# Optimization experiments

Hardware: AMD Instinct MI355X
Metric: run time of the kernel (lower is better)

## Reference

```python
import jax, jax.numpy as jnp
import numpy as np

B, H, W, DIM, HEADS = 4, 32, 32, 768, 12
HD = DIM // HEADS


def setup_inputs() -> dict:
    key = jax.random.key(0)
    ks = jax.random.split(key, 5)
    return {
        "x": jax.random.normal(ks[0], (B, H, W, DIM), jnp.float32),
        "qkv_w": jax.random.normal(ks[1], (3 * DIM, DIM), jnp.float32) * 0.02,
        "qkv_b": jnp.zeros((3 * DIM,), jnp.float32),
        "proj_w": jax.random.normal(ks[2], (DIM, DIM), jnp.float32) * 0.02,
        "proj_b": jnp.zeros((DIM,), jnp.float32),
        "rel_pos_h": jax.random.normal(ks[3], (2 * H - 1, HD), jnp.float32) * 0.02,
        "rel_pos_w": jax.random.normal(ks[4], (2 * W - 1, HD), jnp.float32) * 0.02,
    }


def reference(x, qkv_w, qkv_b, proj_w, proj_b, rel_pos_h, rel_pos_w):
    b, h, w, dim = x.shape
    heads = HEADS
    hd = dim // heads
    n = h * w
    scale = hd ** -0.5

    xf = x.reshape(b, n, dim)
    qkv = xf @ qkv_w.T + qkv_b                          # [b, n, 3*dim]
    qkv = qkv.reshape(b, n, 3, heads, hd)
    qkv = jnp.transpose(qkv, (2, 0, 3, 1, 4)).reshape(3, b * heads, n, hd)
    q, k, v = qkv[0], qkv[1], qkv[2]                    # [b*heads, n, hd]

    # decomposed relative position bias (q_size == k_size, no interpolation)
    idx_h = jnp.arange(h)[:, None] - jnp.arange(h)[None, :] + (h - 1)
    idx_w = jnp.arange(w)[:, None] - jnp.arange(w)[None, :] + (w - 1)
    Rh = rel_pos_h[idx_h]                               # [h, h, hd]
    Rw = rel_pos_w[idx_w]                               # [w, w, hd]
    r_q = q.reshape(b * heads, h, w, hd)
    rel_h = jnp.einsum('bhwc,hkc->bhwk', r_q, Rh)       # [bH, h, w, h]
    rel_w = jnp.einsum('bhwc,wkc->bhwk', r_q, Rw)       # [bH, h, w, w]
    bias = (rel_h[:, :, :, :, None] + rel_w[:, :, :, None, :]).reshape(b * heads, n, n)

    attn = jax.nn.softmax(jnp.einsum('bnd,bmd->bnm', q * scale, k) + bias, axis=-1)
    out = jnp.einsum('bnm,bmd->bnd', attn, v)           # [b*heads, n, hd]
    out = out.reshape(b, heads, n, hd).transpose(0, 2, 1, 3).reshape(b, n, dim)
    out = out @ proj_w.T + proj_b
    return out.reshape(b, h, w, dim)
```

## Files before the change

kernel.cpp:

```cpp
#include <hip/hip_runtime.h>

#define DEV_INLINE static __device__ __forceinline__

typedef __attribute__((ext_vector_type(8))) short bf16x8;
typedef __attribute__((ext_vector_type(4))) float f32x4;
typedef __attribute__((ext_vector_type(16))) float f32x16;

DEV_INLINE unsigned short f2bf(float f) {
  union { float f; unsigned int u; } v; v.f = f;
  unsigned int u = v.u;
  u += 0x7FFFu + ((u >> 16) & 1u);
  return (unsigned short)(u >> 16);
}
DEV_INLINE float bf2f(unsigned short h) {
  union { unsigned int u; float f; } v; v.u = ((unsigned int)h) << 16; return v.f;
}

__global__ __launch_bounds__(256) void cvt_all(const float* __restrict__ x,
                                               const float* __restrict__ qw,
                                               const float* __restrict__ pw,
                                               unsigned short* __restrict__ xb,
                                               unsigned short* __restrict__ wqkv,
                                               unsigned short* __restrict__ wproj) {
  const int bid = blockIdx.x;
  const float* in;
  unsigned short* out;
  int i;
  if (bid < 3072)      { in = x;  out = xb;    i = bid * 256 + threadIdx.x; }
  else if (bid < 4800) { in = qw; out = wqkv;  i = (bid - 3072) * 256 + threadIdx.x; }
  else                 { in = pw; out = wproj; i = (bid - 4800) * 256 + threadIdx.x; }
  float4 v = reinterpret_cast<const float4*>(in)[i];
  ushort4 o;
  o.x = f2bf(v.x); o.y = f2bf(v.y); o.z = f2bf(v.z); o.w = f2bf(v.w);
  reinterpret_cast<ushort4*>(out)[i] = o;
}

template <int MODE>
__global__ __launch_bounds__(256) void gemm_bf16(const unsigned short* __restrict__ A,
                                                 const unsigned short* __restrict__ Bw,
                                                 const float* __restrict__ bias,
                                                 float* __restrict__ outF,
                                                 unsigned short* __restrict__ qo,
                                                 unsigned short* __restrict__ ko,
                                                 unsigned short* __restrict__ vo) {
  __shared__ unsigned short As[3][128 * 32];
  __shared__ unsigned short Bs[3][128 * 32];

  const int tid = threadIdx.x;
  const int lane = tid & 63;
  const int wv = tid >> 6;
  const int wrow = (wv >> 1) * 64;
  const int wcol = (wv & 1) * 64;
  const int m0 = blockIdx.y * 128;
  const int n0 = blockIdx.x * 128;
  const int l15 = lane & 15;
  const int lg = lane >> 4;

  const int srow = lane >> 2;
  const int seg  = (lane & 3) ^ (srow & 3);

  f32x4 acc[4][4];
#pragma unroll
  for (int i = 0; i < 4; ++i)
#pragma unroll
    for (int j = 0; j < 4; ++j) acc[i][j] = (f32x4){0.f, 0.f, 0.f, 0.f};

#define GSTAGE(KT, B)                                                                        \
  do {                                                                                       \
    _Pragma("unroll") for (int pp = 0; pp < 2; ++pp) {                                       \
      int p = wv * 2 + pp;                                   \
      int row = p * 16 + srow;                                                               \
      const unsigned short* ga = &A[(m0 + row) * 768 + (KT) * 32 + seg * 8];                 \
      __builtin_amdgcn_global_load_lds(                                                      \
          (const __attribute__((address_space(1))) unsigned int*)ga,                         \
          (__attribute__((address_space(3))) unsigned int*)&As[B][p * 512], 16, 0, 0);       \
      const unsigned short* gb = &Bw[(n0 + row) * 768 + (KT) * 32 + seg * 8];                \
      __builtin_amdgcn_global_load_lds(                                                      \
          (const __attribute__((address_space(1))) unsigned int*)gb,                         \
          (__attribute__((address_space(3))) unsigned int*)&Bs[B][p * 512], 16, 0, 0);       \
    }                                                                                        \
  } while (0)

  GSTAGE(0, 0);
  GSTAGE(1, 1);

  const int soff = (lg ^ (l15 & 3)) * 8;

#pragma unroll
  for (int kt = 0; kt < 24; ++kt) {
    const int b = kt % 3;
    if (kt < 23) asm volatile("s_waitcnt vmcnt(4)" ::: "memory");
    else         asm volatile("s_waitcnt vmcnt(0)" ::: "memory");
    __builtin_amdgcn_s_barrier();
    asm volatile("" ::: "memory");
    if (kt < 22) GSTAGE(kt + 2, (kt + 2) % 3);

    bf16x8 aF[4], bF[4];
#pragma unroll
    for (int i = 0; i < 4; ++i)
      aF[i] = *reinterpret_cast<const bf16x8*>(&As[b][(wrow + i * 16 + l15) * 32 + soff]);
#pragma unroll
    for (int j = 0; j < 4; ++j)
      bF[j] = *reinterpret_cast<const bf16x8*>(&Bs[b][(wcol + j * 16 + l15) * 32 + soff]);
#pragma unroll
    for (int i = 0; i < 4; ++i)
#pragma unroll
      for (int j = 0; j < 4; ++j)
        acc[i][j] = __builtin_amdgcn_mfma_f32_16x16x32_bf16(aF[i], bF[j], acc[i][j], 0, 0, 0);
  }
#undef GSTAGE

#pragma unroll
  for (int i = 0; i < 4; ++i) {
#pragma unroll
    for (int j = 0; j < 4; ++j) {
#pragma unroll
      for (int r = 0; r < 4; ++r) {
        int row = m0 + wrow + i * 16 + (lane >> 4) * 4 + r;
        int col = n0 + wcol + j * 16 + l15;
        float val = acc[i][j][r] + bias[col];
        if (MODE == 0) {
          int t = col / 768;
          int rem = col - t * 768;
          int head = rem >> 6;
          int c = rem & 63;
          int bb = row >> 10;
          int n = row & 1023;
          if (t == 0) val *= 1.44269504f;
          if (t == 1) val *= 0.125f;
          unsigned short* dst = (t == 0) ? qo : (t == 1) ? ko : vo;
          dst[((bb * 12 + head) * 1024 + n) * 64 + c] = f2bf(val);
        } else {
          outF[row * 768 + col] = val;
        }
      }
    }
  }
}

__global__ __launch_bounds__(256) void vtrans(const unsigned short* __restrict__ vb,
                                              unsigned short* __restrict__ vt) {
  __shared__ unsigned short t[64][72];
  const int n0 = blockIdx.x * 64;
  const int bh = blockIdx.y;
  const int tid = threadIdx.x;
#pragma unroll
  for (int i = 0; i < 4; ++i) {
    int s = tid + i * 256;
    int row = s >> 4, c4 = (s & 15) * 4;
    *reinterpret_cast<ushort4*>(&t[row][c4]) =
        *reinterpret_cast<const ushort4*>(&vb[(bh * 1024 + n0 + row) * 64 + c4]);
  }
  __syncthreads();
#pragma unroll
  for (int i = 0; i < 4; ++i) {
    int s = tid + i * 256;
    int d = s >> 4, n4 = (s & 15) * 4;
    ushort4 o;
    o.x = t[n4 + 0][d]; o.y = t[n4 + 1][d]; o.z = t[n4 + 2][d]; o.w = t[n4 + 3][d];
    *reinterpret_cast<ushort4*>(&vt[(bh * 64 + d) * 1024 + n0 + n4]) = o;
  }
}

DEV_INLINE f32x4 mfma16(bf16x8 a, bf16x8 b, f32x4 c) {
  return __builtin_amdgcn_mfma_f32_16x16x32_bf16(a, b, c, 0, 0, 0);
}

__global__ __launch_bounds__(64) void rel_mfma16(const unsigned short* __restrict__ q,
                                                 const float* __restrict__ rph,
                                                 const float* __restrict__ rpw,
                                                 unsigned short* __restrict__ relwb,
                                                 float* __restrict__ relh) {
  __shared__ unsigned short qs[32 * 72];
  __shared__ unsigned short rhh[32 * 72], rhl[32 * 72];
  __shared__ unsigned short rwh[64 * 72], rwl[64 * 72];
  __shared__ float relh_s[32 * 36];
  __shared__ unsigned short relw_s[32 * 40];

  const int lane = threadIdx.x;
  const int l15 = lane & 15;
  const int lg = lane >> 4;
  const int qh = blockIdx.x;
  const int bh = blockIdx.y;

#pragma unroll
  for (int it = 0; it < 4; ++it) {
    int s = lane + it * 64;
    int row = s >> 3, ch = s & 7;
    *reinterpret_cast<int4*>(&qs[row * 72 + ch * 8]) =
        *reinterpret_cast<const int4*>(&q[(bh * 1024 + qh * 32 + row) * 64 + ch * 8]);
  }
#pragma unroll
  for (int it = 0; it < 8; ++it) {
    int s = lane + it * 64;
    int row = s >> 4, c4 = (s & 15) * 4;
    float4 v = *reinterpret_cast<const float4*>(&rph[(qh + row) * 64 + c4]);
    ushort4 h, l;
    h.x = f2bf(v.x); l.x = f2bf(v.x - bf2f(h.x));
    h.y = f2bf(v.y); l.y = f2bf(v.y - bf2f(h.y));
    h.z = f2bf(v.z); l.z = f2bf(v.z - bf2f(h.z));
    h.w = f2bf(v.w); l.w = f2bf(v.w - bf2f(h.w));
    *reinterpret_cast<ushort4*>(&rhh[row * 72 + c4]) = h;
    *reinterpret_cast<ushort4*>(&rhl[row * 72 + c4]) = l;
  }
#pragma unroll
  for (int it = 0; it < 16; ++it) {
    int s = lane + it * 64;
    int row = s >> 4, c4 = (s & 15) * 4;
    float4 v = (float4){0.f, 0.f, 0.f, 0.f};
    if (row < 63) v = *reinterpret_cast<const float4*>(&rpw[row * 64 + c4]);
    ushort4 h, l;
    h.x = f2bf(v.x); l.x = f2bf(v.x - bf2f(h.x));
    h.y = f2bf(v.y); l.y = f2bf(v.y - bf2f(h.y));
    h.z = f2bf(v.z); l.z = f2bf(v.z - bf2f(h.z));
    h.w = f2bf(v.w); l.w = f2bf(v.w - bf2f(h.w));
    *reinterpret_cast<ushort4*>(&rwh[row * 72 + c4]) = h;
    *reinterpret_cast<ushort4*>(&rwl[row * 72 + c4]) = l;
  }
  __syncthreads();

  const int k0 = lg * 8, k1 = 32 + lg * 8;
  bf16x8 fq[2][2], fhh[2][2], fhl[2][2], fwh[4][2], fwl[4][2];
#pragma unroll
  for (int t = 0; t < 2; ++t) {
    fq[t][0]  = *reinterpret_cast<const bf16x8*>(&qs[(t * 16 + l15) * 72 + k0]);
    fq[t][1]  = *reinterpret_cast<const bf16x8*>(&qs[(t * 16 + l15) * 72 + k1]);
    fhh[t][0] = *reinterpret_cast<const bf16x8*>(&rhh[(t * 16 + l15) * 72 + k0]);
    fhh[t][1] = *reinterpret_cast<const bf16x8*>(&rhh[(t * 16 + l15) * 72 + k1]);
    fhl[t][0] = *reinterpret_cast<const bf16x8*>(&rhl[(t * 16 + l15) * 72 + k0]);
    fhl[t][1] = *reinterpret_cast<const bf16x8*>(&rhl[(t * 16 + l15) * 72 + k1]);
  }
#pragma unroll
  for (int t = 0; t < 4; ++t) {
    fwh[t][0] = *reinterpret_cast<const bf16x8*>(&rwh[(t * 16 + l15) * 72 + k0]);
    fwh[t][1] = *reinterpret_cast<const bf16x8*>(&rwh[(t * 16 + l15) * 72 + k1]);
    fwl[t][0] = *reinterpret_cast<const bf16x8*>(&rwl[(t * 16 + l15) * 72 + k0]);
    fwl[t][1] = *reinterpret_cast<const bf16x8*>(&rwl[(t * 16 + l15) * 72 + k1]);
  }

  f32x4 ah[2][2];
#pragma unroll
  for (int i = 0; i < 2; ++i)
#pragma unroll
    for (int jj = 0; jj < 2; ++jj) {
      f32x4 a = (f32x4){0.f, 0.f, 0.f, 0.f};
      a = mfma16(fhh[i][0], fq[jj][0], a);
      a = mfma16(fhh[i][1], fq[jj][1], a);
      a = mfma16(fhl[i][0], fq[jj][0], a);
      a = mfma16(fhl[i][1], fq[jj][1], a);
      ah[i][jj] = a;
    }
  f32x4 aw[2][4];
#pragma unroll
  for (int i = 0; i < 2; ++i)
#pragma unroll
    for (int jj = 0; jj < 4; ++jj) {
      f32x4 a = (f32x4){0.f, 0.f, 0.f, 0.f};
      a = mfma16(fq[i][0], fwh[jj][0], a);
      a = mfma16(fq[i][1], fwh[jj][1], a);
      a = mfma16(fq[i][0], fwl[jj][0], a);
      a = mfma16(fq[i][1], fwl[jj][1], a);
      aw[i][jj] = a;
    }

#pragma unroll
  for (int i = 0; i < 2; ++i)
#pragma unroll
    for (int jj = 0; jj < 2; ++jj)
#pragma unroll
      for (int r = 0; r < 4; ++r) {
        int t = i * 16 + lg * 4 + r;
        int qw = jj * 16 + l15;
        relh_s[qw * 36 + 31 - t] = ah[i][jj][r];
      }
#pragma unroll
  for (int i = 0; i < 2; ++i)
#pragma unroll
    for (int jj = 0; jj < 4; ++jj)
#pragma unroll
      for (int r = 0; r < 4; ++r) {
        int qw = i * 16 + lg * 4 + r;
        int d = jj * 16 + l15;
        int kw = qw + 31 - d;
        if (kw >= 0 && kw < 32) relw_s[qw * 40 + kw] = f2bf(aw[i][jj][r]);
      }
  __syncthreads();

#pragma unroll
  for (int it = 0; it < 4; ++it) {
    int s = lane + it * 64;
    int row = s >> 3, c4 = (s & 7) * 4;
    *reinterpret_cast<float4*>(&relh[(bh * 1024 + qh * 32 + row) * 32 + c4]) =
        *reinterpret_cast<const float4*>(&relh_s[row * 36 + c4]);
  }
#pragma unroll
  for (int it = 0; it < 2; ++it) {
    int s = lane + it * 64;
    int row = s >> 2, ch = s & 3;
    *reinterpret_cast<int4*>(&relwb[(bh * 1024 + qh * 32 + row) * 32 + ch * 8]) =
        *reinterpret_cast<const int4*>(&relw_s[row * 40 + ch * 8]);
  }
}

DEV_INLINE f32x16 mfma32(bf16x8 a, bf16x8 b, f32x16 c) {
  return __builtin_amdgcn_mfma_f32_32x32x16_bf16(a, b, c, 0, 0, 0);
}

DEV_INLINE bf16x8 make_pa(const float* p) {
  unsigned int W0, W1, W2, W3;
  asm("v_cvt_pk_bf16_f32 %0, %1, %2" : "=v"(W0) : "v"(p[0]), "v"(p[1]));
  asm("v_cvt_pk_bf16_f32 %0, %1, %2" : "=v"(W1) : "v"(p[2]), "v"(p[3]));
  asm("v_cvt_pk_bf16_f32 %0, %1, %2" : "=v"(W2) : "v"(p[4]), "v"(p[5]));
  asm("v_cvt_pk_bf16_f32 %0, %1, %2" : "=v"(W3) : "v"(p[6]), "v"(p[7]));
  asm("v_permlane32_swap_b32 %0, %1" : "+v"(W0), "+v"(W2));
  asm("v_permlane32_swap_b32 %0, %1" : "+v"(W1), "+v"(W3));
  union { unsigned int w[4]; bf16x8 v; } u;
  u.w[0] = W0; u.w[1] = W1; u.w[2] = W2; u.w[3] = W3;
  return u.v;
}

__global__ __launch_bounds__(128) void attn2(const unsigned short* __restrict__ kg,
                                             const unsigned short* __restrict__ vtg,
                                             const unsigned short* __restrict__ qg,
                                             const unsigned short* __restrict__ relwb,
                                             const float* __restrict__ relh,
                                             unsigned short* __restrict__ ao) {
  __shared__ unsigned short k_lin[3][64 * 64];
  __shared__ unsigned short v_lin[3][64 * 64];

  const int tid = threadIdx.x;
  const int lane = tid & 63;
  const int wv = tid >> 6;
  const int l31 = lane & 31;
  const int hi = lane >> 5;

  const int bid = blockIdx.x;
  const int swz = (bid & 7) * 96 + (bid >> 3);
  const int bh = swz >> 4;
  const int qt = swz & 15;
  const int q0 = qt * 64 + wv * 32;

  bf16x8 qf[6];
  {
    const unsigned short* qrow = &qg[(bh * 1024 + q0 + l31) * 64 + hi * 8];
#pragma unroll
    for (int c = 0; c < 4; ++c)
      qf[c] = *reinterpret_cast<const bf16x8*>(&qrow[c * 16]);
    const unsigned short* wrow = &relwb[(bh * 1024 + q0 + l31) * 32 + hi * 8];
    qf[4] = *reinterpret_cast<const bf16x8*>(&wrow[0]);
    qf[5] = *reinterpret_cast<const bf16x8*>(&wrow[16]);
  }

  bf16x8 ohf0, ohf1;
  {
    int t0 = l31 - 8 * hi;
    int t1 = l31 - 16 - 8 * hi;
    union { unsigned int w[4]; bf16x8 v; } u0, u1;
#pragma unroll
    for (int w = 0; w < 4; ++w) {
      u0.w[w] = (t0 >= 0 && (t0 >> 1) == w) ? ((t0 & 1) ? 0x3F800000u : 0x3F80u) : 0u;
      u1.w[w] = (t1 >= 0 && (t1 >> 1) == w) ? ((t1 & 1) ? 0x3F800000u : 0x3F80u) : 0u;
    }
    ohf0 = u0.v; ohf1 = u1.v;
  }

  f32x16 O0, O1;
#pragma unroll
  for (int r = 0; r < 16; ++r) { O0[r] = 0.f; O1[r] = 0.f; }
  float m_r = -3.0e38f, l_r = 0.f;

  const int srow = lane >> 3;
  const int scb = (lane & 7) ^ srow;
  const int rsw = l31 & 7;

#define STAGE(KT, B)                                                                       \
  do {                                                                                     \
    _Pragma("unroll") for (int pp = 0; pp < 4; ++pp) {                                     \
      int p = wv * 4 + pp;                                                                 \
      int row = p * 8 + srow;                                                              \
      const unsigned short* gk = &kg[(bh * 1024 + (KT) * 64 + row) * 64 + scb * 8];        \
      __builtin_amdgcn_global_load_lds(                                                    \
          (const __attribute__((address_space(1))) unsigned int*)gk,                       \
          (__attribute__((address_space(3))) unsigned int*)&k_lin[B][p * 512], 16, 0, 0);  \
      const unsigned short* gv = &vtg[(bh * 64 + row) * 1024 + (KT) * 64 + scb * 8];       \
      __builtin_amdgcn_global_load_lds(                                                    \
          (const __attribute__((address_space(1))) unsigned int*)gv,                       \
          (__attribute__((address_space(3))) unsigned int*)&v_lin[B][p * 512], 16, 0, 0);  \
    }                                                                                      \
  } while (0)

  STAGE(0, 0);
  STAGE(1, 1);

  const float* rhrow = &relh[(bh * 1024 + q0 + l31) * 32];
  float2 bhv = *reinterpret_cast<const float2*>(&rhrow[0]);

  for (int kt = 0; kt < 16; ++kt) {
    const int b = kt % 3;
    if (kt < 15) asm volatile("s_waitcnt vmcnt(8)" ::: "memory");
    else         asm volatile("s_waitcnt vmcnt(0)" ::: "memory");
    __builtin_amdgcn_s_barrier();
    asm volatile("" ::: "memory");
    if (kt < 14) STAGE(kt + 2, (kt + 2) % 3);

    float2 bhv_next = bhv;
    if (kt < 15) bhv_next = *reinterpret_cast<const float2*>(&rhrow[2 * (kt + 1)]);
    float bh0 = bhv.x, bh1 = bhv.y;

    f32x16 s0, s1;
#pragma unroll
    for (int r = 0; r < 16; ++r) { s0[r] = 0.f; s1[r] = 0.f; }
    {
      const unsigned short* kb0 = &k_lin[b][l31 * 64];
      const unsigned short* kb1 = &k_lin[b][(32 + l31) * 64];
      __builtin_amdgcn_s_setprio(1);
#pragma unroll
      for (int c = 0; c < 4; ++c) {
        int cb = ((2 * c + hi) ^ rsw) * 8;
        s0 = mfma32(*reinterpret_cast<const bf16x8*>(&kb0[cb]), qf[c], s0);
        s1 = mfma32(*reinterpret_cast<const bf16x8*>(&kb1[cb]), qf[c], s1);
      }
      s0 = mfma32(ohf0, qf[4], s0);
      s0 = mfma32(ohf1, qf[5], s0);
      s1 = mfma32(ohf0, qf[4], s1);
      s1 = mfma32(ohf1, qf[5], s1);
      __builtin_amdgcn_s_setprio(0);
    }

    float pm0 = s0[0], pm1 = s1[0];
#pragma unroll
    for (int r = 1; r < 16; ++r) { pm0 = fmaxf(pm0, s0[r]); pm1 = fmaxf(pm1, s1[r]); }
    float pmax = fmaxf(pm0 + bh0, pm1 + bh1);
    pmax = fmaxf(pmax, __shfl_xor(pmax, 32));

    if (!__all(pmax <= m_r + 11.5f)) {
      float mnew = fmaxf(m_r, pmax);
      float corr = __builtin_amdgcn_exp2f(m_r - mnew);
      m_r = mnew;
      l_r *= corr;
#pragma unroll
      for (int r = 0; r < 16; ++r) {
        int cr = ((r & 3) + 8 * (r >> 2) + 4 * hi) << 2;
        float c2 = __int_as_float(__builtin_amdgcn_ds_bpermute(cr, __float_as_int(corr)));
        O0[r] *= c2;
        O1[r] *= c2;
      }
    }

    float mb0 = m_r - bh0, mb1 = m_r - bh1;
    float p0[16], p1[16];
    float ps = 0.f;
#pragma unroll
    for (int r = 0; r < 16; ++r) { p0[r] = __builtin_amdgcn_exp2f(s0[r] - mb0); ps += p0[r]; }
#pragma unroll
    for (int r = 0; r < 16; ++r) { p1[r] = __builtin_amdgcn_exp2f(s1[r] - mb1); ps += p1[r]; }
    ps += __shfl_xor(ps, 32);
    l_r += ps;

    bf16x8 pa0 = make_pa(p0 + 0);
    bf16x8 pa1 = make_pa(p0 + 8);
    bf16x8 pa2 = make_pa(p1 + 0);
    bf16x8 pa3 = make_pa(p1 + 8);

    const unsigned short* vb0 = &v_lin[b][l31 * 64];
    const unsigned short* vb1 = &v_lin[b][(32 + l31) * 64];
    __builtin_amdgcn_s_setprio(1);
#pragma unroll
    for (int c = 0; c < 4; ++c) {
      bf16x8 pac = (c == 0) ? pa0 : (c == 1) ? pa1 : (c == 2) ? pa2 : pa3;
      int cb = ((2 * c + hi) ^ rsw) * 8;
      O0 = mfma32(pac, *reinterpret_cast<const bf16x8*>(&vb0[cb]), O0);
      O1 = mfma32(pac, *reinterpret_cast<const bf16x8*>(&vb1[cb]), O1);
    }
    __builtin_amdgcn_s_setprio(0);

    bhv = bhv_next;
  }
#undef STAGE

  float invl = 1.f / l_r;
  const int bb = bh / 12, head = bh % 12;
#pragma unroll
  for (int r = 0; r < 16; ++r) {
    int crow = (r & 3) + 8 * (r >> 2) + 4 * hi;
    float il = __int_as_float(__builtin_amdgcn_ds_bpermute(crow << 2, __float_as_int(invl)));
    int n = q0 + crow;
    unsigned short* dst = &ao[(bb * 1024 + n) * 768 + head * 64];
    dst[l31] = f2bf(O0[r] * il);
    dst[32 + l31] = f2bf(O1[r] * il);
  }
}

extern "C" void kernel_launch(void* const* d_in, const int* in_sizes, int n_in,
                              void* d_out, int out_size, void* d_ws, size_t ws_size,
                              hipStream_t stream) {
  const float* x      = (const float*)d_in[0];
  const float* qkv_w  = (const float*)d_in[1];
  const float* qkv_b  = (const float*)d_in[2];
  const float* proj_w = (const float*)d_in[3];
  const float* proj_b = (const float*)d_in[4];
  const float* rph    = (const float*)d_in[5];
  const float* rpw    = (const float*)d_in[6];
  float* out = (float*)d_out;

  char* ws = (char*)d_ws;
  unsigned short* xb    = (unsigned short*)(ws);
  float*          relh  = (float*)(ws);
  unsigned short* wqkv  = (unsigned short*)(ws + 6291456);
  unsigned short* wproj = (unsigned short*)(ws + 9830400);
  unsigned short* qb    = (unsigned short*)(ws + 11010048);
  unsigned short* kb    = (unsigned short*)(ws + 17301504);
  unsigned short* vb    = (unsigned short*)(ws + 23592960);
  unsigned short* ao    = (unsigned short*)(ws + 23592960);
  unsigned short* vt    = (unsigned short*)(ws + 29884416);
  unsigned short* relwb = (unsigned short*)(ws + 36175872);

  cvt_all<<<5376, 256, 0, stream>>>(x, qkv_w, proj_w, xb, wqkv, wproj);

  gemm_bf16<0><<<dim3(18, 32), 256, 0, stream>>>(xb, wqkv, qkv_b, nullptr, qb, kb, vb);
  vtrans<<<dim3(16, 48), 256, 0, stream>>>(vb, vt);
  rel_mfma16<<<dim3(32, 48), 64, 0, stream>>>(qb, rph, rpw, relwb, relh);
  attn2<<<768, 128, 0, stream>>>(kb, vt, qb, relwb, relh, ao);
  gemm_bf16<1><<<dim3(6, 32), 256, 0, stream>>>(ao, wproj, proj_b, out, nullptr, nullptr, nullptr);
}
```

Before: 110.1 us.

## Software-pipeline QK^T of next tile ahead of softmax in attention loop

Restructures the attention loop so the QK^T MFMAs for tile kt+1 are issued before the softmax and PV work of tile kt. The aim is to overlap matrix-core work with the exp and reduction VALU work. Max and sum reductions become balanced trees to shorten dependency chains. The fine-grained vmcnt(8) waits are replaced by full __syncthreads. This may shrink the effective prefetch depth, and the last iteration does one redundant QK^T.

```diff
diff --git a/kernel.cpp b/kernel.cpp
--- a/kernel.cpp
+++ b/kernel.cpp
@@ -319,6 +319,23 @@
   return u.v;
 }
 
+DEV_INLINE float tree_max16(const float* s) {
+  float a0 = fmaxf(s[0], s[1]),  a1 = fmaxf(s[2], s[3]);
+  float a2 = fmaxf(s[4], s[5]),  a3 = fmaxf(s[6], s[7]);
+  float a4 = fmaxf(s[8], s[9]),  a5 = fmaxf(s[10], s[11]);
+  float a6 = fmaxf(s[12], s[13]), a7 = fmaxf(s[14], s[15]);
+  float b0 = fmaxf(a0, a1), b1 = fmaxf(a2, a3), b2 = fmaxf(a4, a5), b3 = fmaxf(a6, a7);
+  return fmaxf(fmaxf(b0, b1), fmaxf(b2, b3));
+}
+DEV_INLINE float tree_sum16(const float* s) {
+  float a0 = s[0] + s[1],  a1 = s[2] + s[3];
+  float a2 = s[4] + s[5],  a3 = s[6] + s[7];
+  float a4 = s[8] + s[9],  a5 = s[10] + s[11];
+  float a6 = s[12] + s[13], a7 = s[14] + s[15];
+  float b0 = a0 + a1, b1 = a2 + a3, b2 = a4 + a5, b3 = a6 + a7;
+  return (b0 + b1) + (b2 + b3);
+}
+
 __global__ __launch_bounds__(128) void attn2(const unsigned short* __restrict__ kg,
                                              const unsigned short* __restrict__ vtg,
                                              const unsigned short* __restrict__ qg,
@@ -389,47 +406,48 @@
     }                                                                                      \
   } while (0)
 
+#define QKT(BUF, S0, S1)                                                                   \
+  do {                                                                                     \
+    const unsigned short* kb0 = &k_lin[BUF][l31 * 64];                                     \
+    const unsigned short* kb1 = &k_lin[BUF][(32 + l31) * 64];                              \
+    _Pragma("unroll") for (int r = 0; r < 16; ++r) { S0[r] = 0.f; S1[r] = 0.f; }           \
+    __builtin_amdgcn_s_setprio(1);                                                         \
+    _Pragma("unroll") for (int c = 0; c < 4; ++c) {                                        \
+      int cb = ((2 * c + hi) ^ rsw) * 8;                                                   \
+      S0 = mfma32(*reinterpret_cast<const bf16x8*>(&kb0[cb]), qf[c], S0);                  \
+      S1 = mfma32(*reinterpret_cast<const bf16x8*>(&kb1[cb]), qf[c], S1);                  \
+    }                                                                                      \
+    S0 = mfma32(ohf0, qf[4], S0);                                                          \
+    S0 = mfma32(ohf1, qf[5], S0);                                                          \
+    S1 = mfma32(ohf0, qf[4], S1);                                                          \
+    S1 = mfma32(ohf1, qf[5], S1);                                                          \
+    __builtin_amdgcn_s_setprio(0);                                                         \
+  } while (0)
+
   STAGE(0, 0);
   STAGE(1, 1);
+  __syncthreads();
 
   const float* rhrow = &relh[(bh * 1024 + q0 + l31) * 32];
   float2 bhv = *reinterpret_cast<const float2*>(&rhrow[0]);
 
+  f32x16 sc0, sc1;
+  QKT(0, sc0, sc1);
+
   for (int kt = 0; kt < 16; ++kt) {
-    const int b = kt % 3;
-    if (kt < 15) asm volatile("s_waitcnt vmcnt(8)" ::: "memory");
-    else         asm volatile("s_waitcnt vmcnt(0)" ::: "memory");
-    __builtin_amdgcn_s_barrier();
-    asm volatile("" ::: "memory");
+    __syncthreads();
     if (kt < 14) STAGE(kt + 2, (kt + 2) % 3);
 
     float2 bhv_next = bhv;
     if (kt < 15) bhv_next = *reinterpret_cast<const float2*>(&rhrow[2 * (kt + 1)]);
     float bh0 = bhv.x, bh1 = bhv.y;
 
-    f32x16 s0, s1;
-#pragma unroll
-    for (int r = 0; r < 16; ++r) { s0[r] = 0.f; s1[r] = 0.f; }
-    {
-      const unsigned short* kb0 = &k_lin[b][l31 * 64];
-      const unsigned short* kb1 = &k_lin[b][(32 + l31) * 64];
-      __builtin_amdgcn_s_setprio(1);
-#pragma unroll
-      for (int c = 0; c < 4; ++c) {
-        int cb = ((2 * c + hi) ^ rsw) * 8;
-        s0 = mfma32(*reinterpret_cast<const bf16x8*>(&kb0[cb]), qf[c], s0);
-        s1 = mfma32(*reinterpret_cast<const bf16x8*>(&kb1[cb]), qf[c], s1);
-      }
-      s0 = mfma32(ohf0, qf[4], s0);
-      s0 = mfma32(ohf1, qf[5], s0);
-      s1 = mfma32(ohf0, qf[4], s1);
-      s1 = mfma32(ohf1, qf[5], s1);
-      __builtin_amdgcn_s_setprio(0);
-    }
-
-    float pm0 = s0[0], pm1 = s1[0];
-#pragma unroll
-    for (int r = 1; r < 16; ++r) { pm0 = fmaxf(pm0, s0[r]); pm1 = fmaxf(pm1, s1[r]); }
+    const int nb = (kt < 15 ? kt + 1 : 15) % 3;
+    f32x16 sn0, sn1;
+    QKT(nb, sn0, sn1);
+
+    float pm0 = tree_max16((const float*)&sc0);
+    float pm1 = tree_max16((const float*)&sc1);
     float pmax = fmaxf(pm0 + bh0, pm1 + bh1);
     pmax = fmaxf(pmax, __shfl_xor(pmax, 32));
 
@@ -449,11 +467,11 @@
 
     float mb0 = m_r - bh0, mb1 = m_r - bh1;
     float p0[16], p1[16];
-    float ps = 0.f;
-#pragma unroll
-    for (int r = 0; r < 16; ++r) { p0[r] = __builtin_amdgcn_exp2f(s0[r] - mb0); ps += p0[r]; }
-#pragma unroll
-    for (int r = 0; r < 16; ++r) { p1[r] = __builtin_amdgcn_exp2f(s1[r] - mb1); ps += p1[r]; }
+#pragma unroll
+    for (int r = 0; r < 16; ++r) p0[r] = __builtin_amdgcn_exp2f(sc0[r] - mb0);
+#pragma unroll
+    for (int r = 0; r < 16; ++r) p1[r] = __builtin_amdgcn_exp2f(sc1[r] - mb1);
+    float ps = tree_sum16(p0) + tree_sum16(p1);
     ps += __shfl_xor(ps, 32);
     l_r += ps;
 
@@ -462,8 +480,9 @@
     bf16x8 pa2 = make_pa(p1 + 0);
     bf16x8 pa3 = make_pa(p1 + 8);
 
-    const unsigned short* vb0 = &v_lin[b][l31 * 64];
-    const unsigned short* vb1 = &v_lin[b][(32 + l31) * 64];
+    const int vbuf = kt % 3;
+    const unsigned short* vb0 = &v_lin[vbuf][l31 * 64];
+    const unsigned short* vb1 = &v_lin[vbuf][(32 + l31) * 64];
     __builtin_amdgcn_s_setprio(1);
 #pragma unroll
     for (int c = 0; c < 4; ++c) {
@@ -474,8 +493,11 @@
     }
     __builtin_amdgcn_s_setprio(0);
 
+    sc0 = sn0;
+    sc1 = sn1;
     bhv = bhv_next;
   }
+#undef QKT
 #undef STAGE
 
   float invl = 1.f / l_r;
```

Result: no change. 110.8 us (+0.6%).

## Split attention KV range across two wave pairs and merge partial softmax in LDS

Applied to the files above, without the earlier changes.

Each attention block now runs four waves instead of two. Two waves cover the first half of the key tiles and two cover the second half, each with its own double-buffered LDS staging. The partial max, sum and output from the second half are written to shared memory and merged in a flash-decoding style combine. This halves the serial key loop per wave to raise latency hiding and occupancy, at the cost of a reduction epilogue, extra barriers, and replacing the 3-stage vmcnt pipeline with a simpler __syncthreads double buffer. Max and sum reductions are also rewritten as balanced trees to shorten dependency chains.

```diff
diff --git a/kernel.cpp b/kernel.cpp
--- a/kernel.cpp
+++ b/kernel.cpp
@@ -319,18 +319,37 @@
   return u.v;
 }
 
-__global__ __launch_bounds__(128) void attn2(const unsigned short* __restrict__ kg,
+DEV_INLINE float tree_max16(const float* s) {
+  float a0 = fmaxf(s[0], s[1]),  a1 = fmaxf(s[2], s[3]);
+  float a2 = fmaxf(s[4], s[5]),  a3 = fmaxf(s[6], s[7]);
+  float a4 = fmaxf(s[8], s[9]),  a5 = fmaxf(s[10], s[11]);
+  float a6 = fmaxf(s[12], s[13]), a7 = fmaxf(s[14], s[15]);
+  float b0 = fmaxf(a0, a1), b1 = fmaxf(a2, a3), b2 = fmaxf(a4, a5), b3 = fmaxf(a6, a7);
+  return fmaxf(fmaxf(b0, b1), fmaxf(b2, b3));
+}
+DEV_INLINE float tree_sum16(const float* s) {
+  float a0 = s[0] + s[1],  a1 = s[2] + s[3];
+  float a2 = s[4] + s[5],  a3 = s[6] + s[7];
+  float a4 = s[8] + s[9],  a5 = s[10] + s[11];
+  float a6 = s[12] + s[13], a7 = s[14] + s[15];
+  float b0 = a0 + a1, b1 = a2 + a3, b2 = a4 + a5, b3 = a6 + a7;
+  return (b0 + b1) + (b2 + b3);
+}
+
+__global__ __launch_bounds__(256) void attn2(const unsigned short* __restrict__ kg,
                                              const unsigned short* __restrict__ vtg,
                                              const unsigned short* __restrict__ qg,
                                              const unsigned short* __restrict__ relwb,
                                              const float* __restrict__ relh,
                                              unsigned short* __restrict__ ao) {
-  __shared__ unsigned short k_lin[3][64 * 64];
-  __shared__ unsigned short v_lin[3][64 * 64];
+  __shared__ unsigned short k_lin[2][2][64 * 64];
+  __shared__ unsigned short v_lin[2][2][64 * 64];
 
   const int tid = threadIdx.x;
   const int lane = tid & 63;
   const int wv = tid >> 6;
+  const int qh2 = wv & 1;
+  const int kvh = wv >> 1;
   const int l31 = lane & 31;
   const int hi = lane >> 5;
 
@@ -338,7 +357,7 @@
   const int swz = (bid & 7) * 96 + (bid >> 3);
   const int bh = swz >> 4;
   const int qt = swz & 15;
-  const int q0 = qt * 64 + wv * 32;
+  const int q0 = qt * 64 + qh2 * 32;
 
   bf16x8 qf[6];
   {
@@ -373,46 +392,43 @@
   const int scb = (lane & 7) ^ srow;
   const int rsw = l31 & 7;
 
-#define STAGE(KT, B)                                                                       \
-  do {                                                                                     \
-    _Pragma("unroll") for (int pp = 0; pp < 4; ++pp) {                                     \
-      int p = wv * 4 + pp;                                                                 \
-      int row = p * 8 + srow;                                                              \
-      const unsigned short* gk = &kg[(bh * 1024 + (KT) * 64 + row) * 64 + scb * 8];        \
-      __builtin_amdgcn_global_load_lds(                                                    \
-          (const __attribute__((address_space(1))) unsigned int*)gk,                       \
-          (__attribute__((address_space(3))) unsigned int*)&k_lin[B][p * 512], 16, 0, 0);  \
-      const unsigned short* gv = &vtg[(bh * 64 + row) * 1024 + (KT) * 64 + scb * 8];       \
-      __builtin_amdgcn_global_load_lds(                                                    \
-          (const __attribute__((address_space(1))) unsigned int*)gv,                       \
-          (__attribute__((address_space(3))) unsigned int*)&v_lin[B][p * 512], 16, 0, 0);  \
-    }                                                                                      \
+#define STAGE(KT, B)                                                                            \
+  do {                                                                                          \
+    _Pragma("unroll") for (int pp = 0; pp < 4; ++pp) {                                          \
+      int p = qh2 * 4 + pp;                                                                     \
+      int row = p * 8 + srow;                                                                   \
+      const unsigned short* gk = &kg[(bh * 1024 + (KT) * 64 + row) * 64 + scb * 8];             \
+      __builtin_amdgcn_global_load_lds(                                                         \
+          (const __attribute__((address_space(1))) unsigned int*)gk,                            \
+          (__attribute__((address_space(3))) unsigned int*)&k_lin[kvh][B][p * 512], 16, 0, 0);  \
+      const unsigned short* gv = &vtg[(bh * 64 + row) * 1024 + (KT) * 64 + scb * 8];            \
+      __builtin_amdgcn_global_load_lds(                                                         \
+          (const __attribute__((address_space(1))) unsigned int*)gv,                            \
+          (__attribute__((address_space(3))) unsigned int*)&v_lin[kvh][B][p * 512], 16, 0, 0);  \
+    }                                                                                           \
   } while (0)
 
-  STAGE(0, 0);
-  STAGE(1, 1);
+  const int kt0 = kvh * 8;
+  STAGE(kt0, 0);
 
   const float* rhrow = &relh[(bh * 1024 + q0 + l31) * 32];
-  float2 bhv = *reinterpret_cast<const float2*>(&rhrow[0]);
-
-  for (int kt = 0; kt < 16; ++kt) {
-    const int b = kt % 3;
-    if (kt < 15) asm volatile("s_waitcnt vmcnt(8)" ::: "memory");
-    else         asm volatile("s_waitcnt vmcnt(0)" ::: "memory");
-    __builtin_amdgcn_s_barrier();
-    asm volatile("" ::: "memory");
-    if (kt < 14) STAGE(kt + 2, (kt + 2) % 3);
+  float2 bhv = *reinterpret_cast<const float2*>(&rhrow[2 * kt0]);
+
+  for (int lt = 0; lt < 8; ++lt) {
+    const int b = lt & 1;
+    __syncthreads();
+    if (lt < 7) STAGE(kt0 + lt + 1, b ^ 1);
 
     float2 bhv_next = bhv;
-    if (kt < 15) bhv_next = *reinterpret_cast<const float2*>(&rhrow[2 * (kt + 1)]);
+    if (lt < 7) bhv_next = *reinterpret_cast<const float2*>(&rhrow[2 * (kt0 + lt + 1)]);
     float bh0 = bhv.x, bh1 = bhv.y;
 
     f32x16 s0, s1;
 #pragma unroll
     for (int r = 0; r < 16; ++r) { s0[r] = 0.f; s1[r] = 0.f; }
     {
-      const unsigned short* kb0 = &k_lin[b][l31 * 64];
-      const unsigned short* kb1 = &k_lin[b][(32 + l31) * 64];
+      const unsigned short* kb0 = &k_lin[kvh][b][l31 * 64];
+      const unsigned short* kb1 = &k_lin[kvh][b][(32 + l31) * 64];
       __builtin_amdgcn_s_setprio(1);
 #pragma unroll
       for (int c = 0; c < 4; ++c) {
@@ -427,9 +443,8 @@
       __builtin_amdgcn_s_setprio(0);
     }
 
-    float pm0 = s0[0], pm1 = s1[0];
-#pragma unroll
-    for (int r = 1; r < 16; ++r) { pm0 = fmaxf(pm0, s0[r]); pm1 = fmaxf(pm1, s1[r]); }
+    float pm0 = tree_max16((const float*)&s0);
+    float pm1 = tree_max16((const float*)&s1);
     float pmax = fmaxf(pm0 + bh0, pm1 + bh1);
     pmax = fmaxf(pmax, __shfl_xor(pmax, 32));
 
@@ -449,11 +464,11 @@
 
     float mb0 = m_r - bh0, mb1 = m_r - bh1;
     float p0[16], p1[16];
-    float ps = 0.f;
-#pragma unroll
-    for (int r = 0; r < 16; ++r) { p0[r] = __builtin_amdgcn_exp2f(s0[r] - mb0); ps += p0[r]; }
-#pragma unroll
-    for (int r = 0; r < 16; ++r) { p1[r] = __builtin_amdgcn_exp2f(s1[r] - mb1); ps += p1[r]; }
+#pragma unroll
+    for (int r = 0; r < 16; ++r) p0[r] = __builtin_amdgcn_exp2f(s0[r] - mb0);
+#pragma unroll
+    for (int r = 0; r < 16; ++r) p1[r] = __builtin_amdgcn_exp2f(s1[r] - mb1);
+    float ps = tree_sum16(p0) + tree_sum16(p1);
     ps += __shfl_xor(ps, 32);
     l_r += ps;
 
@@ -462,8 +477,8 @@
     bf16x8 pa2 = make_pa(p1 + 0);
     bf16x8 pa3 = make_pa(p1 + 8);
 
-    const unsigned short* vb0 = &v_lin[b][l31 * 64];
-    const unsigned short* vb1 = &v_lin[b][(32 + l31) * 64];
+    const unsigned short* vb0 = &v_lin[kvh][b][l31 * 64];
+    const unsigned short* vb1 = &v_lin[kvh][b][(32 + l31) * 64];
     __builtin_amdgcn_s_setprio(1);
 #pragma unroll
     for (int c = 0; c < 4; ++c) {
@@ -478,16 +493,39 @@
   }
 #undef STAGE
 
-  float invl = 1.f / l_r;
-  const int bb = bh / 12, head = bh % 12;
-#pragma unroll
-  for (int r = 0; r < 16; ++r) {
-    int crow = (r & 3) + 8 * (r >> 2) + 4 * hi;
-    float il = __int_as_float(__builtin_amdgcn_ds_bpermute(crow << 2, __float_as_int(invl)));
-    int n = q0 + crow;
-    unsigned short* dst = &ao[(bb * 1024 + n) * 768 + head * 64];
-    dst[l31] = f2bf(O0[r] * il);
-    dst[32 + l31] = f2bf(O1[r] * il);
+  __syncthreads();
+  float* mb = reinterpret_cast<float*>(&k_lin[0][0][0]);
+  const int base = (qh2 * 64 + lane) * 34;
+  if (kvh == 1) {
+    mb[base + 0] = m_r;
+    mb[base + 1] = l_r;
+#pragma unroll
+    for (int r = 0; r < 16; ++r) { mb[base + 2 + r] = O0[r]; mb[base + 18 + r] = O1[r]; }
+  }
+  __syncthreads();
+  if (kvh == 0) {
+    float m_o = mb[base + 0], l_o = mb[base + 1];
+    float mn = fmaxf(m_r, m_o);
+    float ca = __builtin_amdgcn_exp2f(m_r - mn);
+    float cb = __builtin_amdgcn_exp2f(m_o - mn);
+    l_r = l_r * ca + l_o * cb;
+    float invl = 1.f / l_r;
+
+    const int bb = bh / 12, head = bh % 12;
+#pragma unroll
+    for (int r = 0; r < 16; ++r) {
+      int crow = (r & 3) + 8 * (r >> 2) + 4 * hi;
+      int cri = crow << 2;
+      float car = __int_as_float(__builtin_amdgcn_ds_bpermute(cri, __float_as_int(ca)));
+      float cbr = __int_as_float(__builtin_amdgcn_ds_bpermute(cri, __float_as_int(cb)));
+      float il  = __int_as_float(__builtin_amdgcn_ds_bpermute(cri, __float_as_int(invl)));
+      float o0 = (O0[r] * car + mb[base + 2 + r] * cbr) * il;
+      float o1 = (O1[r] * car + mb[base + 18 + r] * cbr) * il;
+      int n = q0 + crow;
+      unsigned short* dst = &ao[(bb * 1024 + n) * 768 + head * 64];
+      dst[l31] = f2bf(o0);
+      dst[32 + l31] = f2bf(o1);
+    }
   }
 }
 
@@ -520,6 +558,6 @@
   gemm_bf16<0><<<dim3(18, 32), 256, 0, stream>>>(xb, wqkv, qkv_b, nullptr, qb, kb, vb);
   vtrans<<<dim3(16, 48), 256, 0, stream>>>(vb, vt);
   rel_mfma16<<<dim3(32, 48), 64, 0, stream>>>(qb, rph, rpw, relwb, relh);
-  attn2<<<768, 128, 0, stream>>>(kb, vt, qb, relwb, relh, ao);
+  attn2<<<768, 256, 0, stream>>>(kb, vt, qb, relwb, relh, ao);
   gemm_bf16<1><<<dim3(6, 32), 256, 0, stream>>>(ao, wproj, proj_b, out, nullptr, nullptr, nullptr);
 }
```

New measurement: 112.2 us. About the same (+1.9%).

## Run attention block as one wave handling two 32-row query tiles

Applied to the files above, without the earlier changes.

The attention kernel moves from two waves per 64-query block to a single wave that processes both 32-row query halves in turn, reusing each staged K/V tile from LDS. With one wave per block the workgroup barrier goes away, and that wave issues all the global-to-LDS staging loads itself. In exchange the kernel holds twice the accumulators and Q fragments in registers, which may lower occupancy. The grid also has half as many waves, so there is less parallelism to hide latency.

```diff
diff --git a/kernel.cpp b/kernel.cpp
--- a/kernel.cpp
+++ b/kernel.cpp
@@ -319,18 +319,83 @@
   return u.v;
 }
 
-__global__ __launch_bounds__(128) void attn2(const unsigned short* __restrict__ kg,
-                                             const unsigned short* __restrict__ vtg,
-                                             const unsigned short* __restrict__ qg,
-                                             const unsigned short* __restrict__ relwb,
-                                             const float* __restrict__ relh,
-                                             unsigned short* __restrict__ ao) {
+DEV_INLINE void attn_tile(const unsigned short* kb0, const unsigned short* kb1,
+                          const unsigned short* vb0, const unsigned short* vb1,
+                          const bf16x8* qf, bf16x8 ohf0, bf16x8 ohf1,
+                          int hi, int rsw, float bh0, float bh1,
+                          f32x16& O0, f32x16& O1, float& m_r, float& l_r) {
+  f32x16 s0, s1;
+#pragma unroll
+  for (int r = 0; r < 16; ++r) { s0[r] = 0.f; s1[r] = 0.f; }
+  __builtin_amdgcn_s_setprio(1);
+#pragma unroll
+  for (int c = 0; c < 4; ++c) {
+    int cb = ((2 * c + hi) ^ rsw) * 8;
+    s0 = mfma32(*reinterpret_cast<const bf16x8*>(&kb0[cb]), qf[c], s0);
+    s1 = mfma32(*reinterpret_cast<const bf16x8*>(&kb1[cb]), qf[c], s1);
+  }
+  s0 = mfma32(ohf0, qf[4], s0);
+  s0 = mfma32(ohf1, qf[5], s0);
+  s1 = mfma32(ohf0, qf[4], s1);
+  s1 = mfma32(ohf1, qf[5], s1);
+  __builtin_amdgcn_s_setprio(0);
+
+  float pm0 = s0[0], pm1 = s1[0];
+#pragma unroll
+  for (int r = 1; r < 16; ++r) { pm0 = fmaxf(pm0, s0[r]); pm1 = fmaxf(pm1, s1[r]); }
+  float pmax = fmaxf(pm0 + bh0, pm1 + bh1);
+  pmax = fmaxf(pmax, __shfl_xor(pmax, 32));
+
+  if (!__all(pmax <= m_r + 11.5f)) {
+    float mnew = fmaxf(m_r, pmax);
+    float corr = __builtin_amdgcn_exp2f(m_r - mnew);
+    m_r = mnew;
+    l_r *= corr;
+#pragma unroll
+    for (int r = 0; r < 16; ++r) {
+      int cr = ((r & 3) + 8 * (r >> 2) + 4 * hi) << 2;
+      float c2 = __int_as_float(__builtin_amdgcn_ds_bpermute(cr, __float_as_int(corr)));
+      O0[r] *= c2;
+      O1[r] *= c2;
+    }
+  }
+
+  float mb0 = m_r - bh0, mb1 = m_r - bh1;
+  float p0[16], p1[16];
+  float ps = 0.f;
+#pragma unroll
+  for (int r = 0; r < 16; ++r) { p0[r] = __builtin_amdgcn_exp2f(s0[r] - mb0); ps += p0[r]; }
+#pragma unroll
+  for (int r = 0; r < 16; ++r) { p1[r] = __builtin_amdgcn_exp2f(s1[r] - mb1); ps += p1[r]; }
+  ps += __shfl_xor(ps, 32);
+  l_r += ps;
+
+  bf16x8 pa0 = make_pa(p0 + 0);
+  bf16x8 pa1 = make_pa(p0 + 8);
+  bf16x8 pa2 = make_pa(p1 + 0);
+  bf16x8 pa3 = make_pa(p1 + 8);
+
+  __builtin_amdgcn_s_setprio(1);
+#pragma unroll
+  for (int c = 0; c < 4; ++c) {
+    bf16x8 pac = (c == 0) ? pa0 : (c == 1) ? pa1 : (c == 2) ? pa2 : pa3;
+    int cb = ((2 * c + hi) ^ rsw) * 8;
+    O0 = mfma32(pac, *reinterpret_cast<const bf16x8*>(&vb0[cb]), O0);
+    O1 = mfma32(pac, *reinterpret_cast<const bf16x8*>(&vb1[cb]), O1);
+  }
+  __builtin_amdgcn_s_setprio(0);
+}
+
+__global__ __launch_bounds__(64) void attn2(const unsigned short* __restrict__ kg,
+                                            const unsigned short* __restrict__ vtg,
+                                            const unsigned short* __restrict__ qg,
+                                            const unsigned short* __restrict__ relwb,
+                                            const float* __restrict__ relh,
+                                            unsigned short* __restrict__ ao) {
   __shared__ unsigned short k_lin[3][64 * 64];
   __shared__ unsigned short v_lin[3][64 * 64];
 
-  const int tid = threadIdx.x;
-  const int lane = tid & 63;
-  const int wv = tid >> 6;
+  const int lane = threadIdx.x;
   const int l31 = lane & 31;
   const int hi = lane >> 5;
 
@@ -338,17 +403,23 @@
   const int swz = (bid & 7) * 96 + (bid >> 3);
   const int bh = swz >> 4;
   const int qt = swz & 15;
-  const int q0 = qt * 64 + wv * 32;
-
-  bf16x8 qf[6];
+  const int q0 = qt * 64;
+
+  bf16x8 qfA[6], qfB[6];
   {
-    const unsigned short* qrow = &qg[(bh * 1024 + q0 + l31) * 64 + hi * 8];
-#pragma unroll
-    for (int c = 0; c < 4; ++c)
-      qf[c] = *reinterpret_cast<const bf16x8*>(&qrow[c * 16]);
-    const unsigned short* wrow = &relwb[(bh * 1024 + q0 + l31) * 32 + hi * 8];
-    qf[4] = *reinterpret_cast<const bf16x8*>(&wrow[0]);
-    qf[5] = *reinterpret_cast<const bf16x8*>(&wrow[16]);
+    const unsigned short* qrowA = &qg[(bh * 1024 + q0 + l31) * 64 + hi * 8];
+    const unsigned short* qrowB = &qg[(bh * 1024 + q0 + 32 + l31) * 64 + hi * 8];
+#pragma unroll
+    for (int c = 0; c < 4; ++c) {
+      qfA[c] = *reinterpret_cast<const bf16x8*>(&qrowA[c * 16]);
+      qfB[c] = *reinterpret_cast<const bf16x8*>(&qrowB[c * 16]);
+    }
+    const unsigned short* wrowA = &relwb[(bh * 1024 + q0 + l31) * 32 + hi * 8];
+    const unsigned short* wrowB = &relwb[(bh * 1024 + q0 + 32 + l31) * 32 + hi * 8];
+    qfA[4] = *reinterpret_cast<const bf16x8*>(&wrowA[0]);
+    qfA[5] = *reinterpret_cast<const bf16x8*>(&wrowA[16]);
+    qfB[4] = *reinterpret_cast<const bf16x8*>(&wrowB[0]);
+    qfB[5] = *reinterpret_cast<const bf16x8*>(&wrowB[16]);
   }
 
   bf16x8 ohf0, ohf1;
@@ -364,10 +435,10 @@
     ohf0 = u0.v; ohf1 = u1.v;
   }
 
-  f32x16 O0, O1;
-#pragma unroll
-  for (int r = 0; r < 16; ++r) { O0[r] = 0.f; O1[r] = 0.f; }
-  float m_r = -3.0e38f, l_r = 0.f;
+  f32x16 OA0, OA1, OB0, OB1;
+#pragma unroll
+  for (int r = 0; r < 16; ++r) { OA0[r] = 0.f; OA1[r] = 0.f; OB0[r] = 0.f; OB1[r] = 0.f; }
+  float mA = -3.0e38f, lA = 0.f, mB = -3.0e38f, lB = 0.f;
 
   const int srow = lane >> 3;
   const int scb = (lane & 7) ^ srow;
@@ -375,119 +446,76 @@
 
 #define STAGE(KT, B)                                                                       \
   do {                                                                                     \
-    _Pragma("unroll") for (int pp = 0; pp < 4; ++pp) {                                     \
-      int p = wv * 4 + pp;                                                                 \
-      int row = p * 8 + srow;                                                              \
+    _Pragma("unroll") for (int pp = 0; pp < 8; ++pp) {                                     \
+      int row = pp * 8 + srow;                                                             \
       const unsigned short* gk = &kg[(bh * 1024 + (KT) * 64 + row) * 64 + scb * 8];        \
       __builtin_amdgcn_global_load_lds(                                                    \
           (const __attribute__((address_space(1))) unsigned int*)gk,                       \
-          (__attribute__((address_space(3))) unsigned int*)&k_lin[B][p * 512], 16, 0, 0);  \
+          (__attribute__((address_space(3))) unsigned int*)&k_lin[B][pp * 512], 16, 0, 0); \
       const unsigned short* gv = &vtg[(bh * 64 + row) * 1024 + (KT) * 64 + scb * 8];       \
       __builtin_amdgcn_global_load_lds(                                                    \
           (const __attribute__((address_space(1))) unsigned int*)gv,                       \
-          (__attribute__((address_space(3))) unsigned int*)&v_lin[B][p * 512], 16, 0, 0);  \
+          (__attribute__((address_space(3))) unsigned int*)&v_lin[B][pp * 512], 16, 0, 0); \
     }                                                                                      \
   } while (0)
 
   STAGE(0, 0);
   STAGE(1, 1);
 
-  const float* rhrow = &relh[(bh * 1024 + q0 + l31) * 32];
-  float2 bhv = *reinterpret_cast<const float2*>(&rhrow[0]);
+  const float* rhrowA = &relh[(bh * 1024 + q0 + l31) * 32];
+  const float* rhrowB = &relh[(bh * 1024 + q0 + 32 + l31) * 32];
+  float2 bhvA = *reinterpret_cast<const float2*>(&rhrowA[0]);
+  float2 bhvB = *reinterpret_cast<const float2*>(&rhrowB[0]);
 
   for (int kt = 0; kt < 16; ++kt) {
     const int b = kt % 3;
-    if (kt < 15) asm volatile("s_waitcnt vmcnt(8)" ::: "memory");
+    if (kt < 15) asm volatile("s_waitcnt vmcnt(16)" ::: "memory");
     else         asm volatile("s_waitcnt vmcnt(0)" ::: "memory");
-    __builtin_amdgcn_s_barrier();
-    asm volatile("" ::: "memory");
     if (kt < 14) STAGE(kt + 2, (kt + 2) % 3);
 
-    float2 bhv_next = bhv;
-    if (kt < 15) bhv_next = *reinterpret_cast<const float2*>(&rhrow[2 * (kt + 1)]);
-    float bh0 = bhv.x, bh1 = bhv.y;
-
-    f32x16 s0, s1;
-#pragma unroll
-    for (int r = 0; r < 16; ++r) { s0[r] = 0.f; s1[r] = 0.f; }
-    {
-      const unsigned short* kb0 = &k_lin[b][l31 * 64];
-      const unsigned short* kb1 = &k_lin[b][(32 + l31) * 64];
-      __builtin_amdgcn_s_setprio(1);
-#pragma unroll
-      for (int c = 0; c < 4; ++c) {
-        int cb = ((2 * c + hi) ^ rsw) * 8;
-        s0 = mfma32(*reinterpret_cast<const bf16x8*>(&kb0[cb]), qf[c], s0);
-        s1 = mfma32(*reinterpret_cast<const bf16x8*>(&kb1[cb]), qf[c], s1);
-      }
-      s0 = mfma32(ohf0, qf[4], s0);
-      s0 = mfma32(ohf1, qf[5], s0);
-      s1 = mfma32(ohf0, qf[4], s1);
-      s1 = mfma32(ohf1, qf[5], s1);
-      __builtin_amdgcn_s_setprio(0);
-    }
-
-    float pm0 = s0[0], pm1 = s1[0];
-#pragma unroll
-    for (int r = 1; r < 16; ++r) { pm0 = fmaxf(pm0, s0[r]); pm1 = fmaxf(pm1, s1[r]); }
-    float pmax = fmaxf(pm0 + bh0, pm1 + bh1);
-    pmax = fmaxf(pmax, __shfl_xor(pmax, 32));
-
-    if (!__all(pmax <= m_r + 11.5f)) {
-      float mnew = fmaxf(m_r, pmax);
-      float corr = __builtin_amdgcn_exp2f(m_r - mnew);
-      m_r = mnew;
-      l_r *= corr;
-#pragma unroll
-      for (int r = 0; r < 16; ++r) {
-        int cr = ((r & 3) + 8 * (r >> 2) + 4 * hi) << 2;
-        float c2 = __int_as_float(__builtin_amdgcn_ds_bpermute(cr, __float_as_int(corr)));
-        O0[r] *= c2;
-        O1[r] *= c2;
-      }
-    }
-
-    float mb0 = m_r - bh0, mb1 = m_r - bh1;
-    float p0[16], p1[16];
-    float ps = 0.f;
-#pragma unroll
-    for (int r = 0; r < 16; ++r) { p0[r] = __builtin_amdgcn_exp2f(s0[r] - mb0); ps += p0[r]; }
-#pragma unroll
-    for (int r = 0; r < 16; ++r) { p1[r] = __builtin_amdgcn_exp2f(s1[r] - mb1); ps += p1[r]; }
-    ps += __shfl_xor(ps, 32);
-    l_r += ps;
-
-    bf16x8 pa0 = make_pa(p0 + 0);
-    bf16x8 pa1 = make_pa(p0 + 8);
-    bf16x8 pa2 = make_pa(p1 + 0);
-    bf16x8 pa3 = make_pa(p1 + 8);
-
+    float2 bhvA_next = bhvA, bhvB_next = bhvB;
+    if (kt < 15) {
+      bhvA_next = *reinterpret_cast<const float2*>(&rhrowA[2 * (kt + 1)]);
+      bhvB_next = *reinterpret_cast<const float2*>(&rhrowB[2 * (kt + 1)]);
+    }
+
+    const unsigned short* kb0 = &k_lin[b][l31 * 64];
+    const unsigned short* kb1 = &k_lin[b][(32 + l31) * 64];
     const unsigned short* vb0 = &v_lin[b][l31 * 64];
     const unsigned short* vb1 = &v_lin[b][(32 + l31) * 64];
-    __builtin_amdgcn_s_setprio(1);
-#pragma unroll
-    for (int c = 0; c < 4; ++c) {
-      bf16x8 pac = (c == 0) ? pa0 : (c == 1) ? pa1 : (c == 2) ? pa2 : pa3;
-      int cb = ((2 * c + hi) ^ rsw) * 8;
-      O0 = mfma32(pac, *reinterpret_cast<const bf16x8*>(&vb0[cb]), O0);
-      O1 = mfma32(pac, *reinterpret_cast<const bf16x8*>(&vb1[cb]), O1);
-    }
-    __builtin_amdgcn_s_setprio(0);
-
-    bhv = bhv_next;
+
+    attn_tile(kb0, kb1, vb0, vb1, qfA, ohf0, ohf1, hi, rsw, bhvA.x, bhvA.y, OA0, OA1, mA, lA);
+    attn_tile(kb0, kb1, vb0, vb1, qfB, ohf0, ohf1, hi, rsw, bhvB.x, bhvB.y, OB0, OB1, mB, lB);
+
+    bhvA = bhvA_next;
+    bhvB = bhvB_next;
   }
 #undef STAGE
 
-  float invl = 1.f / l_r;
   const int bb = bh / 12, head = bh % 12;
-#pragma unroll
-  for (int r = 0; r < 16; ++r) {
-    int crow = (r & 3) + 8 * (r >> 2) + 4 * hi;
-    float il = __int_as_float(__builtin_amdgcn_ds_bpermute(crow << 2, __float_as_int(invl)));
-    int n = q0 + crow;
-    unsigned short* dst = &ao[(bb * 1024 + n) * 768 + head * 64];
-    dst[l31] = f2bf(O0[r] * il);
-    dst[32 + l31] = f2bf(O1[r] * il);
+  {
+    float invl = 1.f / lA;
+#pragma unroll
+    for (int r = 0; r < 16; ++r) {
+      int crow = (r & 3) + 8 * (r >> 2) + 4 * hi;
+      float il = __int_as_float(__builtin_amdgcn_ds_bpermute(crow << 2, __float_as_int(invl)));
+      int n = q0 + crow;
+      unsigned short* dst = &ao[(bb * 1024 + n) * 768 + head * 64];
+      dst[l31] = f2bf(OA0[r] * il);
+      dst[32 + l31] = f2bf(OA1[r] * il);
+    }
+  }
+  {
+    float invl = 1.f / lB;
+#pragma unroll
+    for (int r = 0; r < 16; ++r) {
+      int crow = (r & 3) + 8 * (r >> 2) + 4 * hi;
+      float il = __int_as_float(__builtin_amdgcn_ds_bpermute(crow << 2, __float_as_int(invl)));
+      int n = q0 + 32 + crow;
+      unsigned short* dst = &ao[(bb * 1024 + n) * 768 + head * 64];
+      dst[l31] = f2bf(OB0[r] * il);
+      dst[32 + l31] = f2bf(OB1[r] * il);
+    }
   }
 }
 
@@ -520,6 +548,6 @@
   gemm_bf16<0><<<dim3(18, 32), 256, 0, stream>>>(xb, wqkv, qkv_b, nullptr, qb, kb, vb);
   vtrans<<<dim3(16, 48), 256, 0, stream>>>(vb, vt);
   rel_mfma16<<<dim3(32, 48), 64, 0, stream>>>(qb, rph, rpw, relwb, relh);
-  attn2<<<768, 128, 0, stream>>>(kb, vt, qb, relwb, relh, ao);
+  attn2<<<768, 64, 0, stream>>>(kb, vt, qb, relwb, relh, ao);
   gemm_bf16<1><<<dim3(6, 32), 256, 0, stream>>>(ao, wproj, proj_b, out, nullptr, nullptr, nullptr);
 }
```

Measured after the change: 122.3 us. 1.11x slower.
